# Kernel optimization log

Hardware: AMD Instinct MI355X
Metric: run time of the kernel (lower is better)

## Reference

```python
import jax, jax.numpy as jnp
import numpy as np

# Representative Blocks2Matrix configuration: single coupled block key
# (l1=2, l2=2, lambda=2), one atom type with 8 radial channels.
N_SYS = 16        # number of systems
N_ATOMS = 64      # atoms per system
L1, L2, LAM = 2, 2, 2
NRAD = 8          # radial channels per (l, Z)
S = 32768         # number of atom-pair samples across all systems
M1, M2, MU = 2 * L1 + 1, 2 * L2 + 1, 2 * LAM + 1
NORB_ATOM = NRAD * M1            # orbitals per atom (radial-major, mu-minor; see make_orbital_map)
N = N_ATOMS * NORB_ATOM          # 2560 orbitals per system


def setup_inputs() -> dict:
    key = jax.random.key(0)
    k1, k2, k3, k4, k5 = jax.random.split(key, 5)
    values = jax.random.normal(k1, (S, MU, NRAD * NRAD), dtype=jnp.float32)
    cg = jax.random.normal(k2, (M1, M2, MU), dtype=jnp.float32)
    sys_idx = jax.random.randint(k3, (S,), 0, N_SYS)
    i_idx = jax.random.randint(k4, (S,), 0, N_ATOMS)
    j_idx = jax.random.randint(k5, (S,), 0, N_ATOMS)
    return {"values": values, "cg": cg, "sys_idx": sys_idx,
            "i_idx": i_idx, "j_idx": j_idx}


def reference(values, cg, sys_idx, i_idx, j_idx):
    # Decouple: uncoupled[s, m1, m2, n1, n2] = sum_mu cg[m1, m2, mu] * values[s, mu, n1, n2]
    vals = values.reshape(S, MU, NRAD, NRAD)
    # orbital ordering is radial-major, mu-minor -> index (n, m)
    blocks = jnp.einsum('abm,smpq->spaqb', cg, vals)  # [S, n1, m1, n2, m2]
    blocks = blocks.reshape(S, NORB_ATOM, NORB_ATOM)
    # Global orbital indices for each pair's block rows/cols
    ar = jnp.arange(NORB_ATOM)
    rows = i_idx[:, None] * NORB_ATOM + ar  # [S, 40]
    cols = j_idx[:, None] * NORB_ATOM + ar  # [S, 40]
    H = jnp.zeros((N_SYS, N, N), dtype=values.dtype)
    # Scatter block at (i, j) and its transpose at (j, i) (Hermitian build)
    H = H.at[sys_idx[:, None, None], rows[:, :, None], cols[:, None, :]].add(blocks)
    H = H.at[sys_idx[:, None, None], cols[:, :, None], rows[:, None, :]].add(
        jnp.swapaxes(blocks, 1, 2))
    return H
```

## Files before the change

kernel.cpp:

```cpp
#include <hip/hip_runtime.h>


#define SS      32768
#define MU      5
#define NORB    40
#define NSYS    16
#define NATOMS  64
#define NDIM    2560
#define NBINS   (NSYS * NATOMS * NATOMS)
#define CAP     16
#define MAXOVF  8192

#define WS_NEEDED   (524288 + (size_t)NBINS * CAP * 4)

__global__ __launch_bounds__(256) void b2m_fill(
    const int* __restrict__ sys_idx, const int* __restrict__ i_idx,
    const int* __restrict__ j_idx,
    int* __restrict__ counts, int* __restrict__ bins,
    int* __restrict__ ovf_cnt, int2* __restrict__ ovf)
{
    int s = blockIdx.x * blockDim.x + threadIdx.x;
    if (s >= SS) return;
    int sy = sys_idx[s], i = i_idx[s], j = j_idx[s];

    int bd = (sy * NATOMS + i) * NATOMS + j;
    int pos = atomicAdd(&counts[bd], 1);
    if (pos < CAP) bins[bd * CAP + pos] = s;
    else { int o = atomicAdd(ovf_cnt, 1); if (o < MAXOVF) ovf[o] = make_int2(bd, s); }

    int bt = (sy * NATOMS + j) * NATOMS + i;
    int st = s | 0x10000;
    pos = atomicAdd(&counts[bt], 1);
    if (pos < CAP) bins[bt * CAP + pos] = st;
    else { int o = atomicAdd(ovf_cnt, 1); if (o < MAXOVF) ovf[o] = make_int2(bt, st); }
}

__global__ __launch_bounds__(320) void b2m_gather(
    const float* __restrict__ values, const float* __restrict__ cg,
    const int* __restrict__ counts, const int* __restrict__ bins,
    float* __restrict__ H)
{
    __shared__ float sv[CAP * 320];
    __shared__ float scg[125];
    __shared__ int   sent[CAP];

    const int bin = blockIdx.x;
    const int tid = threadIdx.x;

    int n = counts[bin];
    if (n > CAP) n = CAP;

    if (tid < 125) scg[tid] = cg[tid];
    if (tid < CAP) sent[tid] = bins[bin * CAP + tid];
    __syncthreads();

    const int kg = tid / 80;
    const int f  = tid - kg * 80;
    for (int u = 0; u < n; u += 4) {
        int k = u + kg;
        if (k < n) {
            int s = sent[k] & 0xFFFF;
            reinterpret_cast<float4*>(sv)[k * 80 + f] =
                reinterpret_cast<const float4*>(values)[s * 80 + f];
        }
    }
    __syncthreads();

    int od[5], ot[5], id_[5], it_[5], rr[5], cc[5];
    #pragma unroll
    for (int it = 0; it < 5; ++it) {
        int e = it * 320 + tid;
        int r = e / 40, c = e - r * 40;
        int p = r / 5, a = r - p * 5;
        int q = c / 5, b = c - q * 5;
        rr[it] = r; cc[it] = c;
        od[it]  = p * 8 + q;
        ot[it]  = q * 8 + p;
        id_[it] = (a * 5 + b) * 5;
        it_[it] = (b * 5 + a) * 5;
    }

    float acc[5] = {0.f, 0.f, 0.f, 0.f, 0.f};
    for (int k = 0; k < n; ++k) {
        const int ent = sent[k];
        const float* vk = sv + k * 320;
        if ((ent & 0x10000) == 0) {
            #pragma unroll
            for (int it = 0; it < 5; ++it)
                #pragma unroll
                for (int m = 0; m < 5; ++m)
                    acc[it] = fmaf(scg[id_[it] + m], vk[m * 64 + od[it]], acc[it]);
        } else {
            #pragma unroll
            for (int it = 0; it < 5; ++it)
                #pragma unroll
                for (int m = 0; m < 5; ++m)
                    acc[it] = fmaf(scg[it_[it] + m], vk[m * 64 + ot[it]], acc[it]);
        }
    }

    const int jj = bin & 63, ii = (bin >> 6) & 63, sy = bin >> 12;
    float* Hs = H + ((size_t)sy * NDIM + (size_t)ii * NORB) * NDIM + (size_t)jj * NORB;
    #pragma unroll
    for (int it = 0; it < 5; ++it)
        Hs[(size_t)rr[it] * NDIM + cc[it]] = acc[it];
}

__global__ __launch_bounds__(256) void b2m_ovf_apply(
    const float* __restrict__ values, const float* __restrict__ cg,
    const int* __restrict__ ovf_cnt, const int2* __restrict__ ovf,
    float* __restrict__ H)
{
    int n = *ovf_cnt;
    if (n > MAXOVF) n = MAXOVF;
    for (int k = blockIdx.x; k < n; k += gridDim.x) {
        int  bin = ovf[k].x;
        int  ent = ovf[k].y;
        int  s   = ent & 0xFFFF;
        bool tr  = (ent >> 16) != 0;
        int  j = bin & 63, i = (bin >> 6) & 63, sy = bin >> 12;
        const float* vs = values + (size_t)s * (MU * 64);
        float* Hs = H + (size_t)sy * NDIM * NDIM;
        for (int e = threadIdx.x; e < 1600; e += blockDim.x) {
            int rr = e / 40, cc = e - rr * 40;
            int R = tr ? cc : rr, C = tr ? rr : cc;
            int p = R / 5, a = R - p * 5;
            int q = C / 5, b = C - q * 5;
            float v = 0.f;
            for (int m = 0; m < 5; ++m)
                v = fmaf(cg[(a * 5 + b) * 5 + m], vs[m * 64 + p * 8 + q], v);
            atomicAdd(Hs + (size_t)(i * NORB + rr) * NDIM + (j * NORB + cc), v);
        }
    }
}

__global__ __launch_bounds__(320) void b2m_scatter(
    const float* __restrict__ values, const float* __restrict__ cg,
    const int* __restrict__ sys_idx, const int* __restrict__ i_idx,
    const int* __restrict__ j_idx, float* __restrict__ H)
{
    __shared__ float sv[MU * 64];
    __shared__ float scg[125];
    const int s = blockIdx.x, tid = threadIdx.x;
    if (tid < MU * 64) sv[tid] = values[(size_t)s * (MU * 64) + tid];
    if (tid < 125) scg[tid] = cg[tid];
    __syncthreads();
    const int sys = sys_idx[s], i = i_idx[s], j = j_idx[s];
    float* Hs = H + (size_t)sys * NDIM * NDIM;
    const int rowbase = i * NORB, colbase = j * NORB;
    #pragma unroll
    for (int it = 0; it < 5; ++it) {
        const int e = tid + it * 320;
        const int r = e / 40, c = e - r * 40;
        const int p = r / 5, a = r - p * 5, q = c / 5, b = c - q * 5;
        float v = 0.f;
        #pragma unroll
        for (int m = 0; m < 5; ++m)
            v = fmaf(scg[(a * 5 + b) * 5 + m], sv[m * 64 + p * 8 + q], v);
        atomicAdd(Hs + (size_t)(rowbase + r) * NDIM + (colbase + c), v);
    }
    #pragma unroll
    for (int it = 0; it < 5; ++it) {
        const int e = tid + it * 320;
        const int c2 = e / 40, r2 = e - c2 * 40;
        const int p = r2 / 5, a = r2 - p * 5, q = c2 / 5, b = c2 - q * 5;
        float v = 0.f;
        #pragma unroll
        for (int m = 0; m < 5; ++m)
            v = fmaf(scg[(a * 5 + b) * 5 + m], sv[m * 64 + p * 8 + q], v);
        atomicAdd(Hs + (size_t)(colbase + c2) * NDIM + (rowbase + r2), v);
    }
}

extern "C" void kernel_launch(void* const* d_in, const int* in_sizes, int n_in,
                              void* d_out, int out_size, void* d_ws, size_t ws_size,
                              hipStream_t stream) {
    const float* values  = (const float*)d_in[0];
    const float* cg      = (const float*)d_in[1];
    const int*   sys_idx = (const int*)d_in[2];
    const int*   i_idx   = (const int*)d_in[3];
    const int*   j_idx   = (const int*)d_in[4];
    float*       H       = (float*)d_out;

    if (ws_size >= WS_NEEDED) {
        char* ws      = (char*)d_ws;
        int*  counts  = (int*)ws;
        int*  ovf_cnt = (int*)(ws + 262144);
        int2* ovf     = (int2*)(ws + 262272);
        int*  bins    = (int*)(ws + 524288);

        hipMemsetAsync(ws, 0, 262400, stream);

        b2m_fill<<<(SS + 255) / 256, 256, 0, stream>>>(
            sys_idx, i_idx, j_idx, counts, bins, ovf_cnt, ovf);
        b2m_gather<<<NBINS, 320, 0, stream>>>(values, cg, counts, bins, H);
        b2m_ovf_apply<<<64, 256, 0, stream>>>(values, cg, ovf_cnt, ovf, H);
    } else {
        hipMemsetAsync(H, 0, (size_t)out_size * sizeof(float), stream);
        b2m_scatter<<<SS, 320, 0, stream>>>(values, cg, sys_idx, i_idx, j_idx, H);
    }
}
```

Measured before the change: 645.5 us.

## Make gather kernel persistent with software-pipelined prefetch of bin lists and values

The gather kernel now launches a fixed grid of blocks, and each block walks a contiguous range of bins instead of handling one bin per block. It double-buffers the first few value slices in shared memory and triple-buffers the bin lists and counts, prefetching the next bin's values and the bin after that's list while computing the current one. Entries past the small shared buffer are read directly from global memory. The aim is to hide global load latency and cut per-block launch and setup cost across the 65536 mostly-sparse bins. The cost is fewer resident blocks, extra synchronization, and possible load imbalance across blocks.

```diff
diff --git a/kernel.cpp b/kernel.cpp
--- a/kernel.cpp
+++ b/kernel.cpp
@@ -9,7 +9,10 @@
 #define NDIM    2560
 #define NBINS   (NSYS * NATOMS * NATOMS)
 #define CAP     16
+#define SC      4
 #define MAXOVF  8192
+#define GBLK    1536
+#define PERB    ((NBINS + GBLK - 1) / GBLK)
 
 #define WS_NEEDED   (524288 + (size_t)NBINS * CAP * 4)
 
@@ -35,75 +38,122 @@
     else { int o = atomicAdd(ovf_cnt, 1); if (o < MAXOVF) ovf[o] = make_int2(bt, st); }
 }
 
+#define ACCUM_DIR(VK)                                                  \
+    _Pragma("unroll")                                                  \
+    for (int it = 0; it < 5; ++it) {                                   \
+        _Pragma("unroll")                                              \
+        for (int m = 0; m < 5; ++m)                                    \
+            acc[it] = fmaf(scg[idd[it] + m], (VK)[m * 64 + od[it]], acc[it]); \
+    }
+#define ACCUM_TR(VK)                                                   \
+    _Pragma("unroll")                                                  \
+    for (int it = 0; it < 5; ++it) {                                   \
+        _Pragma("unroll")                                              \
+        for (int m = 0; m < 5; ++m)                                    \
+            acc[it] = fmaf(scg[idt[it] + m], (VK)[m * 64 + ot[it]], acc[it]); \
+    }
+
 __global__ __launch_bounds__(320) void b2m_gather(
     const float* __restrict__ values, const float* __restrict__ cg,
     const int* __restrict__ counts, const int* __restrict__ bins,
     float* __restrict__ H)
 {
-    __shared__ float sv[CAP * 320];
+    __shared__ float sv[2][SC * 320];
+    __shared__ int   slist[3][CAP];
+    __shared__ int   scnt[3];
     __shared__ float scg[125];
-    __shared__ int   sent[CAP];
-
-    const int bin = blockIdx.x;
+
     const int tid = threadIdx.x;
-
-    int n = counts[bin];
-    if (n > CAP) n = CAP;
+    const int b0  = blockIdx.x * PERB;
+    const int b1  = min(b0 + PERB, NBINS);
+    if (b0 >= NBINS) return;
 
     if (tid < 125) scg[tid] = cg[tid];
-    if (tid < CAP) sent[tid] = bins[bin * CAP + tid];
-    __syncthreads();
-
-    const int kg = tid / 80;
-    const int f  = tid - kg * 80;
-    for (int u = 0; u < n; u += 4) {
-        int k = u + kg;
-        if (k < n) {
-            int s = sent[k] & 0xFFFF;
-            reinterpret_cast<float4*>(sv)[k * 80 + f] =
-                reinterpret_cast<const float4*>(values)[s * 80 + f];
-        }
-    }
-    __syncthreads();
-
-    int od[5], ot[5], id_[5], it_[5], rr[5], cc[5];
+
+    int od[5], ot[5], idd[5], idt[5], soff[5];
     #pragma unroll
     for (int it = 0; it < 5; ++it) {
         int e = it * 320 + tid;
         int r = e / 40, c = e - r * 40;
         int p = r / 5, a = r - p * 5;
         int q = c / 5, b = c - q * 5;
-        rr[it] = r; cc[it] = c;
+        soff[it] = r * NDIM + c;
         od[it]  = p * 8 + q;
         ot[it]  = q * 8 + p;
-        id_[it] = (a * 5 + b) * 5;
-        it_[it] = (b * 5 + a) * 5;
-    }
-
-    float acc[5] = {0.f, 0.f, 0.f, 0.f, 0.f};
-    for (int k = 0; k < n; ++k) {
-        const int ent = sent[k];
-        const float* vk = sv + k * 320;
-        if ((ent & 0x10000) == 0) {
-            #pragma unroll
-            for (int it = 0; it < 5; ++it)
-                #pragma unroll
-                for (int m = 0; m < 5; ++m)
-                    acc[it] = fmaf(scg[id_[it] + m], vk[m * 64 + od[it]], acc[it]);
-        } else {
-            #pragma unroll
-            for (int it = 0; it < 5; ++it)
-                #pragma unroll
-                for (int m = 0; m < 5; ++m)
-                    acc[it] = fmaf(scg[it_[it] + m], vk[m * 64 + ot[it]], acc[it]);
-        }
-    }
-
-    const int jj = bin & 63, ii = (bin >> 6) & 63, sy = bin >> 12;
-    float* Hs = H + ((size_t)sy * NDIM + (size_t)ii * NORB) * NDIM + (size_t)jj * NORB;
-    #pragma unroll
-    for (int it = 0; it < 5; ++it)
-        Hs[(size_t)rr[it] * NDIM + cc[it]] = acc[it];
+        idd[it] = (a * 5 + b) * 5;
+        idt[it] = (b * 5 + a) * 5;
+    }
+
+    const int kq = tid / 80;
+    const int f4 = tid - kq * 80;
+
+    if (tid < CAP) slist[0][tid] = bins[b0 * CAP + tid];
+    if (tid == 317) scnt[0] = min(counts[b0], CAP);
+    if (b0 + 1 < b1) {
+        if (tid < CAP) slist[1][tid] = bins[(b0 + 1) * CAP + tid];
+        if (tid == 318) scnt[1] = min(counts[b0 + 1], CAP);
+    } else if (tid == 318) scnt[1] = 0;
+    __syncthreads();
+
+    {
+        int n0 = scnt[0];
+        if (kq < n0) {
+            int s = slist[0][kq] & 0xFFFF;
+            reinterpret_cast<float4*>(&sv[0][0])[tid] =
+                reinterpret_cast<const float4*>(values)[s * 80 + f4];
+        }
+    }
+
+    for (int t = b0; t < b1; ++t) {
+        const int cur  = (t - b0) & 1;
+        const int s3   = (t - b0) % 3;
+        const int s3n  = (t + 1 - b0) % 3;
+        const int s3nn = (t + 2 - b0) % 3;
+        __syncthreads();
+
+        float4 stg;
+        int n1 = 0;
+        const bool have1 = (t + 1 < b1);
+        if (have1) {
+            n1 = scnt[s3n];
+            if (kq < n1) {
+                int s = slist[s3n][kq] & 0xFFFF;
+                stg = reinterpret_cast<const float4*>(values)[s * 80 + f4];
+            }
+        }
+        int ment = 0, mcnt = 0;
+        const bool have2 = (t + 2 < b1);
+        if (have2) {
+            if (tid < CAP) ment = bins[(t + 2) * CAP + tid];
+            if (tid == 0)  mcnt = counts[t + 2];
+        }
+
+        const int n = scnt[s3];
+        float acc[5] = {0.f, 0.f, 0.f, 0.f, 0.f};
+        for (int k = 0; k < n; ++k) {
+            const int ent = slist[s3][k];
+            if (k < SC) {
+                const float* vk = &sv[cur][k * 320];
+                if ((ent & 0x10000) == 0) { ACCUM_DIR(vk) } else { ACCUM_TR(vk) }
+            } else {
+                const float* vg = values + (size_t)(ent & 0xFFFF) * 320;
+                if ((ent & 0x10000) == 0) { ACCUM_DIR(vg) } else { ACCUM_TR(vg) }
+            }
+        }
+
+        if (have1 && kq < n1)
+            reinterpret_cast<float4*>(&sv[cur ^ 1][0])[tid] = stg;
+        if (have2) {
+            if (tid < CAP) slist[s3nn][tid] = ment;
+            if (tid == 0)  scnt[s3nn] = min(mcnt, CAP);
+        }
+
+        const int jj = t & 63, ii = (t >> 6) & 63, sy = t >> 12;
+        float* Hs = H + ((size_t)sy * NDIM + (size_t)ii * NORB) * NDIM + (size_t)jj * NORB;
+        #pragma unroll
+        for (int it = 0; it < 5; ++it)
+            Hs[soff[it]] = acc[it];
+    }
 }
 
 __global__ __launch_bounds__(256) void b2m_ovf_apply(
@@ -139,10 +189,10 @@
     const int* __restrict__ sys_idx, const int* __restrict__ i_idx,
     const int* __restrict__ j_idx, float* __restrict__ H)
 {
-    __shared__ float sv[MU * 64];
+    __shared__ float svv[MU * 64];
     __shared__ float scg[125];
     const int s = blockIdx.x, tid = threadIdx.x;
-    if (tid < MU * 64) sv[tid] = values[(size_t)s * (MU * 64) + tid];
+    if (tid < MU * 64) svv[tid] = values[(size_t)s * (MU * 64) + tid];
     if (tid < 125) scg[tid] = cg[tid];
     __syncthreads();
     const int sys = sys_idx[s], i = i_idx[s], j = j_idx[s];
@@ -156,7 +206,7 @@
         float v = 0.f;
         #pragma unroll
         for (int m = 0; m < 5; ++m)
-            v = fmaf(scg[(a * 5 + b) * 5 + m], sv[m * 64 + p * 8 + q], v);
+            v = fmaf(scg[(a * 5 + b) * 5 + m], svv[m * 64 + p * 8 + q], v);
         atomicAdd(Hs + (size_t)(rowbase + r) * NDIM + (colbase + c), v);
     }
     #pragma unroll
@@ -167,7 +217,7 @@
         float v = 0.f;
         #pragma unroll
         for (int m = 0; m < 5; ++m)
-            v = fmaf(scg[(a * 5 + b) * 5 + m], sv[m * 64 + p * 8 + q], v);
+            v = fmaf(scg[(a * 5 + b) * 5 + m], svv[m * 64 + p * 8 + q], v);
         atomicAdd(Hs + (size_t)(colbase + c2) * NDIM + (rowbase + r2), v);
     }
 }
@@ -193,7 +243,7 @@
 
         b2m_fill<<<(SS + 255) / 256, 256, 0, stream>>>(
             sys_idx, i_idx, j_idx, counts, bins, ovf_cnt, ovf);
-        b2m_gather<<<NBINS, 320, 0, stream>>>(values, cg, counts, bins, H);
+        b2m_gather<<<GBLK, 320, 0, stream>>>(values, cg, counts, bins, H);
         b2m_ovf_apply<<<64, 256, 0, stream>>>(values, cg, ovf_cnt, ovf, H);
     } else {
         hipMemsetAsync(H, 0, (size_t)out_size * sizeof(float), stream);
```

After: 595.6 us. 1.08x faster.
